# Kernel tuning notes

Hardware: AMD Instinct MI355X
Metric: run time of the kernel (lower is better)

## Reference

```python
import jax, jax.numpy as jnp
import numpy as np

N = 50000   # nodes
E = 800000  # edges
IN = 16     # in_channels
HID = 8     # hidden_channels (per-head)
H = 4       # heads
LAT = 32    # latent_dim
ED = 8      # edge_dim
D1 = H * HID      # 32  (conv1 output, concat)
D2 = H * D1       # 128 (middle conv output, concat)
NEG_SLOPE = 0.2


def setup_inputs() -> dict:
    key = jax.random.key(0)
    ks = jax.random.split(key, 24)
    g = lambda k, shape: jax.random.normal(k, shape, jnp.float32) * 0.1
    inp = {
        'x': jax.random.normal(ks[0], (N, IN), jnp.float32),
        'edge_index': jax.random.randint(ks[1], (2, E), 0, N, jnp.int32),
        'edge_attr': jax.random.normal(ks[2], (E, ED), jnp.float32),
        # conv1: in=16 -> heads=4, out=8 (concat -> 32)
        'Wl1': g(ks[3], (IN, D1)), 'bl1': jnp.zeros((D1,), jnp.float32),
        'Wr1': g(ks[4], (IN, D1)), 'br1': jnp.zeros((D1,), jnp.float32),
        'We1': g(ks[5], (ED, D1)), 'att1': g(ks[6], (H, HID)), 'b1': jnp.zeros((D1,), jnp.float32),
        # middle conv: in=32 -> heads=4, out=32 (concat -> 128), residual linear
        'Wl2': g(ks[7], (D1, D2)), 'bl2': jnp.zeros((D2,), jnp.float32),
        'Wr2': g(ks[8], (D1, D2)), 'br2': jnp.zeros((D2,), jnp.float32),
        'We2': g(ks[9], (ED, D2)), 'att2': g(ks[10], (H, D1)), 'b2': jnp.zeros((D2,), jnp.float32),
        'Rw2': g(ks[11], (D1, D2)),
        # conv_final: in=128 -> heads=1, out=32
        'Wl3': g(ks[12], (D2, LAT)), 'bl3': jnp.zeros((LAT,), jnp.float32),
        'Wr3': g(ks[13], (D2, LAT)), 'br3': jnp.zeros((LAT,), jnp.float32),
        'We3': g(ks[14], (ED, LAT)), 'att3': g(ks[15], (1, LAT)), 'b3': jnp.zeros((LAT,), jnp.float32),
    }
    return inp


def _segment_softmax(logits, seg, n):
    # logits: [E, H], seg: [E] target-node ids
    m = jax.lax.stop_gradient(jax.ops.segment_max(logits, seg, num_segments=n))
    e = jnp.exp(logits - m[seg])
    s = jax.ops.segment_sum(e, seg, num_segments=n)
    return e / s[seg]


def _gatv2_layer(x, src, dst, eattr, Wl, bl, Wr, br, We, att, bias, heads, out_ch, n, resW=None):
    # GATv2Conv (eval mode, concat=True): message = xl[src]*alpha,
    # alpha from LeakyReLU(xl[src] + xr[dst] + We@edge_attr) . att, edge-softmax over dst.
    xl = (x @ Wl + bl).reshape(n, heads, out_ch)
    xr = (x @ Wr + br).reshape(n, heads, out_ch)
    e = (eattr @ We).reshape(-1, heads, out_ch)
    m = xl[src] + xr[dst] + e                      # [E, H, C]
    s = jax.nn.leaky_relu(m, NEG_SLOPE)
    logits = jnp.einsum('ehc,hc->eh', s, att)      # [E, H]
    alpha = _segment_softmax(logits, dst, n)       # [E, H]
    out = jax.ops.segment_sum(alpha[:, :, None] * xl[src], dst, num_segments=n)
    out = out.reshape(n, heads * out_ch) + bias
    if resW is not None:
        out = out + x @ resW
    return out


def reference(x, edge_index, edge_attr, Wl1, bl1, Wr1, br1, We1, att1, b1,
              Wl2, bl2, Wr2, br2, We2, att2, b2, Rw2,
              Wl3, bl3, Wr3, br3, We3, att3, b3):
    src, dst = edge_index[0], edge_index[1]
    # add_self_loops with fill_value='mean': loop edge_attr = mean of incoming edge_attr
    ones = jnp.ones((src.shape[0],), x.dtype)
    deg = jax.ops.segment_sum(ones, dst, num_segments=N)
    loop_attr = jax.ops.segment_sum(edge_attr, dst, num_segments=N) / jnp.maximum(deg, 1.0)[:, None]
    loop = jnp.arange(N, dtype=src.dtype)
    s2 = jnp.concatenate([src, loop])
    d2 = jnp.concatenate([dst, loop])
    ea = jnp.concatenate([edge_attr, loop_attr], axis=0)

    h = jax.nn.relu(_gatv2_layer(x, s2, d2, ea, Wl1, bl1, Wr1, br1, We1, att1, b1, H, HID, N))
    h = jax.nn.relu(_gatv2_layer(h, s2, d2, ea, Wl2, bl2, Wr2, br2, We2, att2, b2, H, D1, N, resW=Rw2))
    out = _gatv2_layer(h, s2, d2, ea, Wl3, bl3, Wr3, br3, We3, att3, b3, 1, LAT, N)
    return out
```

## Files before the change

### kernel.cpp

```cpp
#include <hip/hip_runtime.h>
#include <hip/hip_fp16.h>

#define NEG_SLOPE 0.2f

constexpr int NN = 50000;
constexpr int EE = 800000;

static inline int cdiv(int a, int b) { return (a + b - 1) / b; }

typedef _Float16 h2 __attribute__((ext_vector_type(2)));

#if __has_builtin(__builtin_amdgcn_fdot2)
static __device__ inline float fdot2f(h2 a, h2 b, float c) {
    return __builtin_amdgcn_fdot2(a, b, c, false);
}
#else
static __device__ inline float fdot2f(h2 a, h2 b, float c) {
    return c + (float)a.x * (float)b.x + (float)a.y * (float)b.y;
}
#endif

static __device__ inline h2 bch2(unsigned u) { return __builtin_bit_cast(h2, u); }

struct __align__(16) ERec {
    __half ea[8];
    int src;
    int pad[3];
};

__global__ void hist_kernel(const int4* __restrict__ dst4, int* __restrict__ rowcnt, int E4) {
    int t = blockIdx.x * blockDim.x + threadIdx.x;
    if (t >= E4) return;
    int4 d = dst4[t];
    atomicAdd(&rowcnt[d.x], 1);
    atomicAdd(&rowcnt[d.y], 1);
    atomicAdd(&rowcnt[d.z], 1);
    atomicAdd(&rowcnt[d.w], 1);
}

__global__ void scana_kernel(const int* __restrict__ cnt, int* __restrict__ blocksum, int n) {
    __shared__ int s[256];
    int t = threadIdx.x, g = blockIdx.x * 256 + t;
    s[t] = (g < n) ? cnt[g] + 1 : 0;
    __syncthreads();
    for (int off = 128; off > 0; off >>= 1) {
        if (t < off) s[t] += s[t + off];
        __syncthreads();
    }
    if (t == 0) blocksum[blockIdx.x] = s[0];
}

__global__ void scanb_kernel(const int* __restrict__ cnt, const int* __restrict__ blocksum,
                             int nbk, int* __restrict__ rowptr, int* __restrict__ cursor,
                             ERec* __restrict__ csr, int n) {
    __shared__ int bs[256];
    __shared__ int s[256];
    int t = threadIdx.x;
    bs[t] = (t < nbk) ? blocksum[t] : 0;
    __syncthreads();
    for (int off = 1; off < 256; off <<= 1) {
        int tv = (t >= off) ? bs[t - off] : 0; __syncthreads();
        bs[t] += tv; __syncthreads();
    }
    int blockoff = (blockIdx.x > 0) ? bs[blockIdx.x - 1] : 0;
    int g = blockIdx.x * 256 + t;
    int val = (g < n) ? cnt[g] + 1 : 0;
    s[t] = val; __syncthreads();
    for (int off = 1; off < 256; off <<= 1) {
        int tv = (t >= off) ? s[t - off] : 0; __syncthreads();
        s[t] += tv; __syncthreads();
    }
    if (g >= n) return;
    int incl = s[t] + blockoff;
    rowptr[g + 1] = incl;
    int beg = incl - val;
    cursor[g] = beg + 1;
    csr[beg].src = g;
    if (g == 0) rowptr[0] = 0;
}

__global__ void scatter_kernel(const int* __restrict__ src, const int* __restrict__ dst,
                               const float* __restrict__ eattr,
                               int* __restrict__ cursor, ERec* __restrict__ csr, int E) {
    int t = blockIdx.x * blockDim.x + threadIdx.x;
    if (t >= E) return;
    int d = dst[t];
    int pos = atomicAdd(&cursor[d], 1);
    const float4* ea4 = (const float4*)(eattr + (size_t)t * 8);
    float4 a = ea4[0], b = ea4[1];
    __half2 h0 = __floats2half2_rn(a.x, a.y);
    __half2 h1 = __floats2half2_rn(a.z, a.w);
    __half2 h2v = __floats2half2_rn(b.x, b.y);
    __half2 h3 = __floats2half2_rn(b.z, b.w);
    uint4 u;
    u.x = *(unsigned*)&h0; u.y = *(unsigned*)&h1;
    u.z = *(unsigned*)&h2v; u.w = *(unsigned*)&h3;
    ERec* r = &csr[pos];
    *(uint4*)r->ea = u;
    r->src = src[t];
}

template <int NB1>
__global__ __launch_bounds__(256) void fused_nl1_loopsea_kernel(
    const float* __restrict__ x,
    const float* __restrict__ Wl, const float* __restrict__ bl,
    const float* __restrict__ Wr, const float* __restrict__ br,
    __half* __restrict__ xl, __half* __restrict__ xr,
    const int* __restrict__ rowptr, ERec* __restrict__ csr, int n) {
    constexpr int K = 16, CT = 32, NPB = 8;
    __shared__ float Wls[K * CT];
    __shared__ float Wrs[K * CT];
    __shared__ float xs[NPB * K];
    int tid = threadIdx.x;
    if (blockIdx.x < NB1) {
        int ty = tid >> 5, c = tid & 31;
        for (int i = tid; i < K * CT; i += 256) { Wls[i] = Wl[i]; Wrs[i] = Wr[i]; }
        int node0 = blockIdx.x * NPB;
        for (int i = tid; i < NPB * K; i += 256) {
            int nd = node0 + i / K;
            xs[i] = (nd < n) ? x[(size_t)node0 * K + i] : 0.f;
        }
        __syncthreads();
        int node = node0 + ty;
        if (node >= n) return;
        float aL = bl[c], aR = br[c];
        const float* xrow = &xs[ty * K];
        for (int k = 0; k < K; ++k) {
            float xv = xrow[k];
            aL = fmaf(xv, Wls[k * CT + c], aL);
            aR = fmaf(xv, Wrs[k * CT + c], aR);
        }
        xl[(size_t)node * CT + c] = __float2half(aL);
        xr[(size_t)node * CT + c] = __float2half(aR);
    } else {
        int wave = ((blockIdx.x - NB1) * 256 + tid) >> 6;
        int lane = tid & 63;
        if (wave >= n) return;
        int beg = rowptr[wave], end = rowptr[wave + 1];
        int k = lane & 7, j0 = lane >> 3;
        float s = 0.f;
        for (int j = beg + 1 + j0; j < end; j += 8)
            s += __half2float(csr[j].ea[k]);
        s += __shfl_xor(s, 8); s += __shfl_xor(s, 16); s += __shfl_xor(s, 32);
        int cnt = end - beg - 1;
        if (lane < 8) csr[beg].ea[lane] = __float2half(s / fmaxf((float)cnt, 1.f));
    }
}

template <int K, int CT>
__global__ __launch_bounds__(256) void node_linear_h_kernel(
    const __half* __restrict__ x,
    const float* __restrict__ Wl, const float* __restrict__ bl,
    const float* __restrict__ Wr, const float* __restrict__ br,
    __half* __restrict__ xl, __half* __restrict__ xr, int n) {
    constexpr int NPB = 256 / CT;
    constexpr int K2 = K / 2;
    __shared__ h2 Wls[K2 * CT];
    __shared__ h2 Wrs[K2 * CT];
    __shared__ h2 xs[NPB * K2];
    int tid = threadIdx.y * CT + threadIdx.x;
    for (int i = tid; i < K2 * CT; i += 256) {
        int k2 = i / CT, c = i % CT;
        Wls[i] = h2{(_Float16)Wl[(2 * k2) * CT + c], (_Float16)Wl[(2 * k2 + 1) * CT + c]};
        Wrs[i] = h2{(_Float16)Wr[(2 * k2) * CT + c], (_Float16)Wr[(2 * k2 + 1) * CT + c]};
    }
    int node0 = blockIdx.x * NPB;
    const unsigned* xg = (const unsigned*)(x + (size_t)node0 * K);
    for (int i = tid; i < NPB * K2; i += 256) {
        int nd = node0 + i / K2;
        unsigned u = (nd < n) ? xg[i] : 0u;
        xs[i] = bch2(u);
    }
    __syncthreads();
    int node = node0 + threadIdx.y;
    if (node >= n) return;
    int c = threadIdx.x;
    float aL = bl[c], aR = br[c];
    const h2* xrow = &xs[threadIdx.y * K2];
    for (int k = 0; k < K2; ++k) {
        h2 xv = xrow[k];
        aL = fdot2f(xv, Wls[k * CT + c], aL);
        aR = fdot2f(xv, Wrs[k * CT + c], aR);
    }
    xl[(size_t)node * CT + c] = __float2half(aL);
    xr[(size_t)node * CT + c] = __float2half(aR);
}

template <bool RELU, bool RES>
__global__ __launch_bounds__(256) void agg128_kernel(
    const int* __restrict__ rowptr, const ERec* __restrict__ csr,
    const __half* __restrict__ xl, const __half* __restrict__ xr,
    const float* __restrict__ We,
    const float* __restrict__ att,
    const float* __restrict__ bias,
    const __half* __restrict__ hres,
    const float* __restrict__ Rw,
    __half* __restrict__ out, int n) {
    __shared__ float Rws[RES ? 32 * 128 : 1];
    int tid = threadIdx.x;
    if (RES) {
        for (int i = tid; i < 32 * 128; i += 256) Rws[i] = Rw[i];
        __syncthreads();
    }
    int node = (blockIdx.x * 256 + tid) >> 6;
    int lane = tid & 63;
    if (node >= n) return;
    int sub = lane >> 5, cl = lane & 31;
    int c0 = 4 * cl;
    h2 wch[4][4];
    float attc[4];
#pragma unroll
    for (int c = 0; c < 4; ++c) {
        attc[c] = att[c0 + c];
#pragma unroll
        for (int k = 0; k < 4; ++k)
            wch[c][k] = h2{(_Float16)We[(2 * k) * 128 + c0 + c],
                           (_Float16)We[(2 * k + 1) * 128 + c0 + c]};
    }
    int beg = rowptr[node], end = rowptr[node + 1];
    uint2 xru = *(const uint2*)&xr[(size_t)node * 128 + c0];
    h2 xr01 = bch2(xru.x), xr23 = bch2(xru.y);
    float xrc[4] = {(float)xr01.x, (float)xr01.y, (float)xr23.x, (float)xr23.y};
    float num[4] = {0.f, 0.f, 0.f, 0.f};
    float den = 0.f;

    int j = beg + sub;
    uint4 uA, uB; int sA, sB; uint2 xA, xB;
    if (j < end) {
        uA = *(const uint4*)csr[j].ea; sA = csr[j].src;
        xA = *(const uint2*)&xl[(size_t)sA * 128 + c0];
    }
    if (j + 2 < end) {
        uB = *(const uint4*)csr[j + 2].ea; sB = csr[j + 2].src;
        xB = *(const uint2*)&xl[(size_t)sB * 128 + c0];
    }
    while (j < end) {
        int jf = j + 4;
        uint4 uC; int sC; uint2 xC;
        if (jf < end) {
            uC = *(const uint4*)csr[jf].ea; sC = csr[jf].src;
            xC = *(const uint2*)&xl[(size_t)sC * 128 + c0];
        }
        h2 e0 = bch2(uA.x), e1 = bch2(uA.y), e2 = bch2(uA.z), e3 = bch2(uA.w);
        h2 xl01 = bch2(xA.x), xl23 = bch2(xA.y);
        float xls[4] = {(float)xl01.x, (float)xl01.y, (float)xl23.x, (float)xl23.y};
        float p = 0.f;
#pragma unroll
        for (int c = 0; c < 4; ++c) {
            float m = xls[c] + xrc[c];
            m = fdot2f(e0, wch[c][0], m); m = fdot2f(e1, wch[c][1], m);
            m = fdot2f(e2, wch[c][2], m); m = fdot2f(e3, wch[c][3], m);
            float sv = fmaxf(m, 0.f) + NEG_SLOPE * fminf(m, 0.f);
            p = fmaf(sv, attc[c], p);
        }
        p += __shfl_xor(p, 1); p += __shfl_xor(p, 2); p += __shfl_xor(p, 4);
        float wgt = __expf(p);
#pragma unroll
        for (int c = 0; c < 4; ++c) num[c] = fmaf(wgt, xls[c], num[c]);
        den += wgt;
        j += 2;
        uA = uB; sA = sB; xA = xB;
        uB = uC; sB = sC; xB = xC;
    }
#pragma unroll
    for (int c = 0; c < 4; ++c) num[c] += __shfl_xor(num[c], 32);
    den += __shfl_xor(den, 32);
    if (sub == 0) {
        float inv = 1.f / den;
        float v[4];
#pragma unroll
        for (int c = 0; c < 4; ++c) v[c] = num[c] * inv + bias[c0 + c];
        if (RES) {
            float hr = __half2float(hres[(size_t)node * 32 + cl]);
#pragma unroll
            for (int k = 0; k < 32; ++k) {
                float hv = __shfl(hr, k, 32);
                float4 rw = *(const float4*)&Rws[k * 128 + c0];
                v[0] = fmaf(hv, rw.x, v[0]); v[1] = fmaf(hv, rw.y, v[1]);
                v[2] = fmaf(hv, rw.z, v[2]); v[3] = fmaf(hv, rw.w, v[3]);
            }
        }
        if (RELU) {
#pragma unroll
            for (int c = 0; c < 4; ++c) v[c] = fmaxf(v[c], 0.f);
        }
        __half2 o01 = __floats2half2_rn(v[0], v[1]);
        __half2 o23 = __floats2half2_rn(v[2], v[3]);
        uint2 ou; ou.x = *(unsigned*)&o01; ou.y = *(unsigned*)&o23;
        *(uint2*)&out[(size_t)node * 128 + c0] = ou;
    }
}

template <int HC, bool RELU, typename OUT>
__global__ __launch_bounds__(256) void agg32_kernel(
    const int* __restrict__ rowptr, const ERec* __restrict__ csr,
    const __half* __restrict__ xl, const __half* __restrict__ xr,
    const float* __restrict__ We,
    const float* __restrict__ att,
    const float* __restrict__ bias,
    OUT* __restrict__ out, int n) {
    int tid = threadIdx.x;
    int node = (blockIdx.x * 256 + tid) >> 4;
    int q = tid & 15;
    if (node >= n) return;
    int c0 = 2 * q;
    h2 wc0[4], wc1[4];
#pragma unroll
    for (int k = 0; k < 4; ++k) {
        wc0[k] = h2{(_Float16)We[(2 * k) * 32 + c0], (_Float16)We[(2 * k + 1) * 32 + c0]};
        wc1[k] = h2{(_Float16)We[(2 * k) * 32 + c0 + 1], (_Float16)We[(2 * k + 1) * 32 + c0 + 1]};
    }
    float att0 = att[c0], att1 = att[c0 + 1];
    int beg = rowptr[node], end = rowptr[node + 1];
    h2 xrh = bch2(*(const unsigned*)&xr[(size_t)node * 32 + c0]);
    float xrc0 = (float)xrh.x, xrc1 = (float)xrh.y;
    float num0 = 0.f, num1 = 0.f, den = 0.f;

    int j = beg;
    uint4 uA, uB, uC; int sA, sB, sC; unsigned xA, xB, xC;
    if (j < end) {
        uA = *(const uint4*)csr[j].ea; sA = csr[j].src;
        xA = *(const unsigned*)&xl[(size_t)sA * 32 + c0];
    }
    if (j + 1 < end) {
        uB = *(const uint4*)csr[j + 1].ea; sB = csr[j + 1].src;
        xB = *(const unsigned*)&xl[(size_t)sB * 32 + c0];
    }
    if (j + 2 < end) {
        uC = *(const uint4*)csr[j + 2].ea; sC = csr[j + 2].src;
        xC = *(const unsigned*)&xl[(size_t)sC * 32 + c0];
    }
    while (j < end) {
        int jf = j + 3;
        uint4 uD; int sD; unsigned xD;
        if (jf < end) {
            uD = *(const uint4*)csr[jf].ea; sD = csr[jf].src;
            xD = *(const unsigned*)&xl[(size_t)sD * 32 + c0];
        }
        h2 e0 = bch2(uA.x), e1 = bch2(uA.y), e2 = bch2(uA.z), e3 = bch2(uA.w);
        h2 xlh = bch2(xA);
        float xls0 = (float)xlh.x, xls1 = (float)xlh.y;
        float m0 = xls0 + xrc0, m1 = xls1 + xrc1;
        m0 = fdot2f(e0, wc0[0], m0); m0 = fdot2f(e1, wc0[1], m0);
        m0 = fdot2f(e2, wc0[2], m0); m0 = fdot2f(e3, wc0[3], m0);
        m1 = fdot2f(e0, wc1[0], m1); m1 = fdot2f(e1, wc1[1], m1);
        m1 = fdot2f(e2, wc1[2], m1); m1 = fdot2f(e3, wc1[3], m1);
        float s0 = fmaxf(m0, 0.f) + NEG_SLOPE * fminf(m0, 0.f);
        float s1 = fmaxf(m1, 0.f) + NEG_SLOPE * fminf(m1, 0.f);
        float p = fmaf(s0, att0, s1 * att1);
#pragma unroll
        for (int off = HC / 4; off > 0; off >>= 1) p += __shfl_xor(p, off);
        float wgt = __expf(p);
        num0 = fmaf(wgt, xls0, num0);
        num1 = fmaf(wgt, xls1, num1);
        den += wgt;
        j += 1;
        uA = uB; sA = sB; xA = xB;
        uB = uC; sB = sC; xB = xC;
        uC = uD; sC = sD; xC = xD;
    }
    float inv = 1.f / den;
    float v0 = num0 * inv + bias[c0];
    float v1 = num1 * inv + bias[c0 + 1];
    if (RELU) { v0 = fmaxf(v0, 0.f); v1 = fmaxf(v1, 0.f); }
    if constexpr (sizeof(OUT) == 2) {
        __half2 o = __floats2half2_rn(v0, v1);
        *(__half2*)&out[(size_t)node * 32 + c0] = o;
    } else {
        float2 o; o.x = v0; o.y = v1;
        *(float2*)&out[(size_t)node * 32 + c0] = o;
    }
}

extern "C" void kernel_launch(void* const* d_in, const int* in_sizes, int n_in,
                              void* d_out, int out_size, void* d_ws, size_t ws_size,
                              hipStream_t stream) {
    const float* x    = (const float*)d_in[0];
    const int* ei     = (const int*)d_in[1];
    const float* eatt = (const float*)d_in[2];
    const float* Wl1 = (const float*)d_in[3],  *bl1 = (const float*)d_in[4];
    const float* Wr1 = (const float*)d_in[5],  *br1 = (const float*)d_in[6];
    const float* We1 = (const float*)d_in[7],  *att1 = (const float*)d_in[8];
    const float* b1  = (const float*)d_in[9];
    const float* Wl2 = (const float*)d_in[10], *bl2 = (const float*)d_in[11];
    const float* Wr2 = (const float*)d_in[12], *br2 = (const float*)d_in[13];
    const float* We2 = (const float*)d_in[14], *att2 = (const float*)d_in[15];
    const float* b2  = (const float*)d_in[16], *Rw2 = (const float*)d_in[17];
    const float* Wl3 = (const float*)d_in[18], *bl3 = (const float*)d_in[19];
    const float* Wr3 = (const float*)d_in[20], *br3 = (const float*)d_in[21];
    const float* We3 = (const float*)d_in[22], *att3 = (const float*)d_in[23];
    const float* b3  = (const float*)d_in[24];

    const int* srcp = ei;
    const int* dstp = ei + EE;

    char* w = (char*)d_ws;
    size_t off = 0;
    auto alloc = [&](size_t bytes) { char* p = w + off; off += (bytes + 255) & ~size_t(255); return p; };
    int*    rowcnt   = (int*)alloc((size_t)NN * 4);
    int*    rowptr   = (int*)alloc((size_t)(NN + 1) * 4);
    int*    cursor   = (int*)alloc((size_t)NN * 4);
    int*    blocksum = (int*)alloc(256 * 4);
    ERec*   csr      = (ERec*)alloc((size_t)(EE + NN) * sizeof(ERec));
    __half* xlbuf    = (__half*)alloc((size_t)NN * 128 * 2);
    __half* xrbuf    = (__half*)alloc((size_t)NN * 128 * 2);
    __half* hA       = (__half*)alloc((size_t)NN * 32 * 2);
    __half* hB       = (__half*)alloc((size_t)NN * 128 * 2);

    int nb = cdiv(NN, 256);

    hipMemsetAsync(rowcnt, 0, (size_t)NN * 4, stream);
    hist_kernel<<<cdiv(EE / 4, 256), 256, 0, stream>>>((const int4*)dstp, rowcnt, EE / 4);
    scana_kernel<<<nb, 256, 0, stream>>>(rowcnt, blocksum, NN);
    scanb_kernel<<<nb, 256, 0, stream>>>(rowcnt, blocksum, nb, rowptr, cursor, csr, NN);
    scatter_kernel<<<cdiv(EE, 256), 256, 0, stream>>>(
        srcp, dstp, eatt, cursor, csr, EE);

    constexpr int NB1 = (NN + 7) / 8;
    int nb_ls = cdiv(NN, 4);
    fused_nl1_loopsea_kernel<NB1><<<NB1 + nb_ls, 256, 0, stream>>>(
        x, Wl1, bl1, Wr1, br1, xlbuf, xrbuf, rowptr, csr, NN);

    agg32_kernel<8, true, __half><<<cdiv(NN, 16), 256, 0, stream>>>(
        rowptr, csr, xlbuf, xrbuf, We1, att1, b1, hA, NN);

    node_linear_h_kernel<32, 128><<<cdiv(NN, 2), dim3(128, 2), 0, stream>>>(
        hA, Wl2, bl2, Wr2, br2, xlbuf, xrbuf, NN);
    agg128_kernel<true, true><<<cdiv(NN, 4), 256, 0, stream>>>(
        rowptr, csr, xlbuf, xrbuf, We2, att2, b2, hA, Rw2, hB, NN);

    node_linear_h_kernel<128, 32><<<cdiv(NN, 8), dim3(32, 8), 0, stream>>>(
        hB, Wl3, bl3, Wr3, br3, xlbuf, xrbuf, NN);
    agg32_kernel<32, false, float><<<cdiv(NN, 16), 256, 0, stream>>>(
        rowptr, csr, xlbuf, xrbuf, We3, att3, b3,
        (float*)d_out, NN);
}
```

Baseline: 468.0 us.

## Move residual linear into node-linear kernel and deepen CSR prefetch pipeline

The residual projection x@Rw2 plus bias is now computed in a new node-linear kernel alongside xl/xr and written as fp16 into the output buffer. The aggregation kernel reads it back as its base value, which drops the per-block shared-memory load of Rw and the 32-step shuffle loop. Both aggregation kernels also restructure their edge prefetch: edge records are fetched further ahead, and the dependent xl gather is issued one step ahead using the already-loaded source index. The trade-offs are an extra fp16 round-trip of the residual, which costs some precision, and a larger shared-memory footprint in the node-linear kernel.

```diff
diff --git a/kernel.cpp b/kernel.cpp
--- a/kernel.cpp
+++ b/kernel.cpp
@@ -186,6 +186,51 @@
     xr[(size_t)node * CT + c] = __float2half(aR);
 }
 
+__global__ __launch_bounds__(256) void nlh2_res_kernel(
+    const __half* __restrict__ x,
+    const float* __restrict__ Wl, const float* __restrict__ bl,
+    const float* __restrict__ Wr, const float* __restrict__ br,
+    const float* __restrict__ Rw,
+    const float* __restrict__ b2,
+    __half* __restrict__ xl, __half* __restrict__ xr,
+    __half* __restrict__ res, int n) {
+    constexpr int K = 32, CT = 128, NPB = 2, K2 = K / 2;
+    __shared__ h2 Wls[K2 * CT];
+    __shared__ h2 Wrs[K2 * CT];
+    __shared__ float Rws[K * CT];
+    __shared__ h2 xs[NPB * K2];
+    int tid = threadIdx.y * CT + threadIdx.x;
+    for (int i = tid; i < K2 * CT; i += 256) {
+        int k2 = i / CT, c = i % CT;
+        Wls[i] = h2{(_Float16)Wl[(2 * k2) * CT + c], (_Float16)Wl[(2 * k2 + 1) * CT + c]};
+        Wrs[i] = h2{(_Float16)Wr[(2 * k2) * CT + c], (_Float16)Wr[(2 * k2 + 1) * CT + c]};
+    }
+    for (int i = tid; i < K * CT; i += 256) Rws[i] = Rw[i];
+    int node0 = blockIdx.x * NPB;
+    const unsigned* xg = (const unsigned*)(x + (size_t)node0 * K);
+    for (int i = tid; i < NPB * K2; i += 256) {
+        int nd = node0 + i / K2;
+        unsigned u = (nd < n) ? xg[i] : 0u;
+        xs[i] = bch2(u);
+    }
+    __syncthreads();
+    int node = node0 + threadIdx.y;
+    if (node >= n) return;
+    int c = threadIdx.x;
+    float aL = bl[c], aR = br[c], aS = b2[c];
+    const h2* xrow = &xs[threadIdx.y * K2];
+    for (int k = 0; k < K2; ++k) {
+        h2 xv = xrow[k];
+        aL = fdot2f(xv, Wls[k * CT + c], aL);
+        aR = fdot2f(xv, Wrs[k * CT + c], aR);
+        aS = fmaf((float)xv.x, Rws[(2 * k) * CT + c], aS);
+        aS = fmaf((float)xv.y, Rws[(2 * k + 1) * CT + c], aS);
+    }
+    xl[(size_t)node * CT + c] = __float2half(aL);
+    xr[(size_t)node * CT + c] = __float2half(aR);
+    res[(size_t)node * CT + c] = __float2half(aS);
+}
+
 template <bool RELU, bool RES>
 __global__ __launch_bounds__(256) void agg128_kernel(
     const int* __restrict__ rowptr, const ERec* __restrict__ csr,
@@ -193,15 +238,8 @@
     const float* __restrict__ We,
     const float* __restrict__ att,
     const float* __restrict__ bias,
-    const __half* __restrict__ hres,
-    const float* __restrict__ Rw,
     __half* __restrict__ out, int n) {
-    __shared__ float Rws[RES ? 32 * 128 : 1];
     int tid = threadIdx.x;
-    if (RES) {
-        for (int i = tid; i < 32 * 128; i += 256) Rws[i] = Rw[i];
-        __syncthreads();
-    }
     int node = (blockIdx.x * 256 + tid) >> 6;
     int lane = tid & 63;
     if (node >= n) return;
@@ -225,24 +263,17 @@
     float den = 0.f;
 
     int j = beg + sub;
-    uint4 uA, uB; int sA, sB; uint2 xA, xB;
-    if (j < end) {
-        uA = *(const uint4*)csr[j].ea; sA = csr[j].src;
-        xA = *(const uint2*)&xl[(size_t)sA * 128 + c0];
-    }
-    if (j + 2 < end) {
-        uB = *(const uint4*)csr[j + 2].ea; sB = csr[j + 2].src;
-        xB = *(const uint2*)&xl[(size_t)sB * 128 + c0];
-    }
+    uint4 u0, u1, u2; int s0, s1, s2; uint2 x0;
+    if (j < end)     { u0 = *(const uint4*)csr[j].ea;     s0 = csr[j].src; }
+    if (j + 2 < end) { u1 = *(const uint4*)csr[j + 2].ea; s1 = csr[j + 2].src; }
+    if (j + 4 < end) { u2 = *(const uint4*)csr[j + 4].ea; s2 = csr[j + 4].src; }
+    if (j < end)     x0 = *(const uint2*)&xl[(size_t)s0 * 128 + c0];
     while (j < end) {
-        int jf = j + 4;
-        uint4 uC; int sC; uint2 xC;
-        if (jf < end) {
-            uC = *(const uint4*)csr[jf].ea; sC = csr[jf].src;
-            xC = *(const uint2*)&xl[(size_t)sC * 128 + c0];
-        }
-        h2 e0 = bch2(uA.x), e1 = bch2(uA.y), e2 = bch2(uA.z), e3 = bch2(uA.w);
-        h2 xl01 = bch2(xA.x), xl23 = bch2(xA.y);
+        uint4 uT; int sT; uint2 xT;
+        if (j + 6 < end) { uT = *(const uint4*)csr[j + 6].ea; sT = csr[j + 6].src; }
+        if (j + 2 < end) { xT = *(const uint2*)&xl[(size_t)s1 * 128 + c0]; }
+        h2 e0 = bch2(u0.x), e1 = bch2(u0.y), e2 = bch2(u0.z), e3 = bch2(u0.w);
+        h2 xl01 = bch2(x0.x), xl23 = bch2(x0.y);
         float xls[4] = {(float)xl01.x, (float)xl01.y, (float)xl23.x, (float)xl23.y};
         float p = 0.f;
 #pragma unroll
@@ -259,27 +290,28 @@
         for (int c = 0; c < 4; ++c) num[c] = fmaf(wgt, xls[c], num[c]);
         den += wgt;
         j += 2;
-        uA = uB; sA = sB; xA = xB;
-        uB = uC; sB = sC; xB = xC;
+        u0 = u1; u1 = u2; u2 = uT;
+        s1 = s2; s2 = sT;
+        x0 = xT;
     }
 #pragma unroll
     for (int c = 0; c < 4; ++c) num[c] += __shfl_xor(num[c], 32);
     den += __shfl_xor(den, 32);
     if (sub == 0) {
         float inv = 1.f / den;
+        float base[4];
+        if (RES) {
+            uint2 ru = *(const uint2*)&out[(size_t)node * 128 + c0];
+            h2 r01 = bch2(ru.x), r23 = bch2(ru.y);
+            base[0] = (float)r01.x; base[1] = (float)r01.y;
+            base[2] = (float)r23.x; base[3] = (float)r23.y;
+        } else {
+#pragma unroll
+            for (int c = 0; c < 4; ++c) base[c] = bias[c0 + c];
+        }
         float v[4];
 #pragma unroll
-        for (int c = 0; c < 4; ++c) v[c] = num[c] * inv + bias[c0 + c];
-        if (RES) {
-            float hr = __half2float(hres[(size_t)node * 32 + cl]);
-#pragma unroll
-            for (int k = 0; k < 32; ++k) {
-                float hv = __shfl(hr, k, 32);
-                float4 rw = *(const float4*)&Rws[k * 128 + c0];
-                v[0] = fmaf(hv, rw.x, v[0]); v[1] = fmaf(hv, rw.y, v[1]);
-                v[2] = fmaf(hv, rw.z, v[2]); v[3] = fmaf(hv, rw.w, v[3]);
-            }
-        }
+        for (int c = 0; c < 4; ++c) v[c] = fmaf(num[c], inv, base[c]);
         if (RELU) {
 #pragma unroll
             for (int c = 0; c < 4; ++c) v[c] = fmaxf(v[c], 0.f);
@@ -317,37 +349,26 @@
     float num0 = 0.f, num1 = 0.f, den = 0.f;
 
     int j = beg;
-    uint4 uA, uB, uC; int sA, sB, sC; unsigned xA, xB, xC;
-    if (j < end) {
-        uA = *(const uint4*)csr[j].ea; sA = csr[j].src;
-        xA = *(const unsigned*)&xl[(size_t)sA * 32 + c0];
-    }
-    if (j + 1 < end) {
-        uB = *(const uint4*)csr[j + 1].ea; sB = csr[j + 1].src;
-        xB = *(const unsigned*)&xl[(size_t)sB * 32 + c0];
-    }
-    if (j + 2 < end) {
-        uC = *(const uint4*)csr[j + 2].ea; sC = csr[j + 2].src;
-        xC = *(const unsigned*)&xl[(size_t)sC * 32 + c0];
-    }
+    uint4 u0, u1, u2; int s0, s1, s2; unsigned x0;
+    if (j < end)     { u0 = *(const uint4*)csr[j].ea;     s0 = csr[j].src; }
+    if (j + 1 < end) { u1 = *(const uint4*)csr[j + 1].ea; s1 = csr[j + 1].src; }
+    if (j + 2 < end) { u2 = *(const uint4*)csr[j + 2].ea; s2 = csr[j + 2].src; }
+    if (j < end)     x0 = *(const unsigned*)&xl[(size_t)s0 * 32 + c0];
     while (j < end) {
-        int jf = j + 3;
-        uint4 uD; int sD; unsigned xD;
-        if (jf < end) {
-            uD = *(const uint4*)csr[jf].ea; sD = csr[jf].src;
-            xD = *(const unsigned*)&xl[(size_t)sD * 32 + c0];
-        }
-        h2 e0 = bch2(uA.x), e1 = bch2(uA.y), e2 = bch2(uA.z), e3 = bch2(uA.w);
-        h2 xlh = bch2(xA);
+        uint4 uT; int sT; unsigned xT;
+        if (j + 3 < end) { uT = *(const uint4*)csr[j + 3].ea; sT = csr[j + 3].src; }
+        if (j + 1 < end) { xT = *(const unsigned*)&xl[(size_t)s1 * 32 + c0]; }
+        h2 e0 = bch2(u0.x), e1 = bch2(u0.y), e2 = bch2(u0.z), e3 = bch2(u0.w);
+        h2 xlh = bch2(x0);
         float xls0 = (float)xlh.x, xls1 = (float)xlh.y;
         float m0 = xls0 + xrc0, m1 = xls1 + xrc1;
         m0 = fdot2f(e0, wc0[0], m0); m0 = fdot2f(e1, wc0[1], m0);
         m0 = fdot2f(e2, wc0[2], m0); m0 = fdot2f(e3, wc0[3], m0);
         m1 = fdot2f(e0, wc1[0], m1); m1 = fdot2f(e1, wc1[1], m1);
         m1 = fdot2f(e2, wc1[2], m1); m1 = fdot2f(e3, wc1[3], m1);
-        float s0 = fmaxf(m0, 0.f) + NEG_SLOPE * fminf(m0, 0.f);
-        float s1 = fmaxf(m1, 0.f) + NEG_SLOPE * fminf(m1, 0.f);
-        float p = fmaf(s0, att0, s1 * att1);
+        float s0v = fmaxf(m0, 0.f) + NEG_SLOPE * fminf(m0, 0.f);
+        float s1v = fmaxf(m1, 0.f) + NEG_SLOPE * fminf(m1, 0.f);
+        float p = fmaf(s0v, att0, s1v * att1);
 #pragma unroll
         for (int off = HC / 4; off > 0; off >>= 1) p += __shfl_xor(p, off);
         float wgt = __expf(p);
@@ -355,9 +376,9 @@
         num1 = fmaf(wgt, xls1, num1);
         den += wgt;
         j += 1;
-        uA = uB; sA = sB; xA = xB;
-        uB = uC; sB = sC; xB = xC;
-        uC = uD; sC = sD; xC = xD;
+        u0 = u1; u1 = u2; u2 = uT;
+        s1 = s2; s2 = sT;
+        x0 = xT;
     }
     float inv = 1.f / den;
     float v0 = num0 * inv + bias[c0];
@@ -424,10 +445,10 @@
     agg32_kernel<8, true, __half><<<cdiv(NN, 16), 256, 0, stream>>>(
         rowptr, csr, xlbuf, xrbuf, We1, att1, b1, hA, NN);
 
-    node_linear_h_kernel<32, 128><<<cdiv(NN, 2), dim3(128, 2), 0, stream>>>(
-        hA, Wl2, bl2, Wr2, br2, xlbuf, xrbuf, NN);
+    nlh2_res_kernel<<<cdiv(NN, 2), dim3(128, 2), 0, stream>>>(
+        hA, Wl2, bl2, Wr2, br2, Rw2, b2, xlbuf, xrbuf, hB, NN);
     agg128_kernel<true, true><<<cdiv(NN, 4), 256, 0, stream>>>(
-        rowptr, csr, xlbuf, xrbuf, We2, att2, b2, hA, Rw2, hB, NN);
+        rowptr, csr, xlbuf, xrbuf, We2, att2, b2, hB, NN);
 
     node_linear_h_kernel<128, 32><<<cdiv(NN, 8), dim3(32, 8), 0, stream>>>(
         hB, Wl3, bl3, Wr3, br3, xlbuf, xrbuf, NN);
```

Result: no change. 468.6 us (+0.1%).
